# Performance work log

Measured on AMD Instinct MI355X. Metric: run time of the kernel, lower is better.

The kernel has to match this reference:

```python
import jax, jax.numpy as jnp
import numpy as np

INPUT_DIM = 16
LW = 128          # layerwidth
NB_LAYERS = 4
NB_X = 4096
NB_THETA = 128
PARAM_COUNT = INPUT_DIM * LW + LW + (NB_LAYERS - 1) * (LW * LW + LW) + LW + 1  # 51841


def setup_inputs() -> dict:
    k1, k2 = jax.random.split(jax.random.key(0))
    x = jax.random.normal(k1, (NB_X, INPUT_DIM), dtype=jnp.float32)
    theta = jax.random.normal(k2, (NB_THETA, PARAM_COUNT), dtype=jnp.float32)
    return {"x": x, "theta": theta}


def reference(x, theta):
    # x: [nb_x, input_dim], theta: [nb_theta, param_count]
    t = theta.shape[0]
    off = 0
    # first layer: W0 [t, LW, INPUT_DIM], b0 [t, LW]
    W0 = theta[:, off:off + INPUT_DIM * LW].reshape(t, LW, INPUT_DIM); off += INPUT_DIM * LW
    b0 = theta[:, off:off + LW]; off += LW
    h = jnp.tanh(jnp.einsum('thi,xi->txh', W0, x) + b0[:, None, :])  # [t, nb_x, LW]
    # hidden layers
    for _ in range(NB_LAYERS - 1):
        W = theta[:, off:off + LW * LW].reshape(t, LW, LW); off += LW * LW
        b = theta[:, off:off + LW]; off += LW
        h = jnp.tanh(jnp.einsum('tho,txo->txh', W, h) + b[:, None, :])
    # output layer: Wl [t, LW], bl [t, 1]
    Wl = theta[:, off:off + LW]; off += LW
    bl = theta[:, off:off + 1]
    out = jnp.einsum('th,txh->tx', Wl, h)[..., None] + bl[:, None, :]  # [t, nb_x, 1]
    return out
```

## Files before the change

kernel.cpp:

```cpp
#include <hip/hip_runtime.h>


#define IND      16
#define THREADS  1024
#define PARAMS   51841
#define SCALE    2.8853900817779268f

#define WS_W0    12582912
#define WS_SC    (WS_W0 + 128 * 8192)
#define WS_X     (WS_SC + 128 * 4096)
#define WS_XLO   (WS_X + 131072)
#define WS_TOTAL (WS_X + 262144)


#define LDS_B    98304
#define LDS_WL   (LDS_B + 1536)
#define LDS_SZ   (LDS_B + 2064)

typedef _Float16 f16x8 __attribute__((ext_vector_type(8)));
typedef _Float16 f16x4 __attribute__((ext_vector_type(4)));
typedef float    f32x16 __attribute__((ext_vector_type(16)));
typedef float    f32x4v __attribute__((ext_vector_type(4)));
typedef unsigned u32x2  __attribute__((ext_vector_type(2)));

union U4 { unsigned u[4]; f16x8 v; };

__device__ __forceinline__ unsigned tanh2pk(float z0, float z1) {
    const float e0 = __builtin_amdgcn_exp2f(z0);
    const float e1 = __builtin_amdgcn_exp2f(z1);
    const float y0 = __builtin_fmaf(__builtin_amdgcn_rcpf(1.0f + e0), -2.0f, 1.0f);
    const float y1 = __builtin_fmaf(__builtin_amdgcn_rcpf(1.0f + e1), -2.0f, 1.0f);
    return __builtin_bit_cast(unsigned, __builtin_amdgcn_cvt_pkrtz(y0, y1));
}

#define MFMA(A, B, C) __builtin_amdgcn_mfma_f32_32x32x16_f16((A), (B), (C), 0, 0, 0)

__device__ __forceinline__ void gload16(const void* g, void* l) {
    __builtin_amdgcn_global_load_lds(
        (const __attribute__((address_space(1))) void*)g,
        (__attribute__((address_space(3))) void*)l, 16, 0, 0);
}

__device__ __forceinline__ void conv8(const float* __restrict__ s, char* hidst,
                                      char* lodst, float scale) {
    float v[8];
    *reinterpret_cast<float4*>(v)     = *reinterpret_cast<const float4*>(s);
    *reinterpret_cast<float4*>(v + 4) = *reinterpret_cast<const float4*>(s + 4);
    f16x8 hi, lo;
#pragma unroll
    for (int i = 0; i < 8; ++i) {
        const float sv = v[i] * scale;
        hi[i] = (_Float16)sv;
        lo[i] = (_Float16)(sv - (float)hi[i]);
    }
    *reinterpret_cast<f16x8*>(hidst) = hi;
    *reinterpret_cast<f16x8*>(lodst) = lo;
}

__global__ __launch_bounds__(256)
void prep_kernel(const float* __restrict__ theta, const float* __restrict__ xin,
                 char* __restrict__ ws)
{
    const int b = blockIdx.x, tid = threadIdx.x;
    if (b < 3072) {
        const int t = b / 24, rem = b % 24, li = rem >> 3, hblk = rem & 7;
        const int h  = hblk * 16 + (tid >> 4);
        const int kc = (tid >> 1) & 7, kh = tid & 1;
        const float* src = theta + (size_t)t * PARAMS + 2176 + li * 16512
                         + h * 128 + kc * 16 + kh * 8;
        float v[8];
        *reinterpret_cast<float4*>(v)     = *reinterpret_cast<const float4*>(src);
        *reinterpret_cast<float4*>(v + 4) = *reinterpret_cast<const float4*>(src + 4);
        f16x8 p;
#pragma unroll
        for (int i = 0; i < 8; ++i) p[i] = (_Float16)(v[i] * SCALE);
        char* img = ws + ((size_t)(t * 3 + li) << 15);
        *reinterpret_cast<f16x8*>(img + ((h >> 5) * 8 + kc) * 1024
                                      + (kh * 32 + (h & 31)) * 16) = p;
    } else if (b < 3136) {
        const int gid = (b - 3072) * 256 + tid;
        const int t = gid >> 7, h = gid & 127;
        const float* src = theta + (size_t)t * PARAMS + h * IND;
        char* dst = ws + WS_W0 + (size_t)t * 8192 + h * 32;
        conv8(src,     dst,      dst + 4096,      SCALE);
        conv8(src + 8, dst + 16, dst + 4096 + 16, SCALE);
    } else if (b < 3264) {
        const int t = b - 3136;
        const float* th = theta + (size_t)t * PARAMS;
        float* base = reinterpret_cast<float*>(ws + WS_SC + (size_t)t * 4096);
        if (tid < 128) base[tid] = SCALE * th[2048 + tid];
        for (int k = tid; k < 384; k += 256)
            base[128 + k] = SCALE * th[2176 + (k >> 7) * 16512 + 16384 + (k & 127)];
        if (tid < 128) base[512 + tid] = th[51712 + tid];
        if (tid == 0)  base[640] = th[51840];
    } else {
        const int row = (b - 3264) * 256 + tid;
        const float* src = xin + (size_t)row * IND;
        char* hid = ws + WS_X   + (size_t)row * 32;
        char* lod = ws + WS_XLO + (size_t)row * 32;
        conv8(src,     hid,      lod,      1.0f);
        conv8(src + 8, hid + 16, lod + 16, 1.0f);
    }
}

__global__ __launch_bounds__(THREADS, 4)
void mlp_main(const char* __restrict__ ws, float* __restrict__ out)
{
    __shared__ __align__(16) char sL[LDS_SZ];

    const int tid = threadIdx.x, bid = blockIdx.x;
    const int sw  = (bid & 7) * 128 + (bid >> 3);
    const int t   = sw >> 3, xt = sw & 7;
    const int lane = tid & 63, w = tid >> 6, r31 = lane & 31, khalf = lane >> 5;
    const int bpa  = (lane ^ 32) << 2;
    (void)bpa;

    const float* __restrict__ wsc = reinterpret_cast<const float*>(
        ws + WS_SC + (size_t)t * 4096);

    {
        const char* img = ws + ((size_t)(t * 3) << 15);
#pragma unroll
        for (int c = 0; c < 6; ++c) {
            const int o = (c * 1024 + tid) * 16;
            gload16(img + o, sL + o);
        }
    }
    if (tid < 513)
        *reinterpret_cast<float*>(sL + LDS_B + tid * 4) = wsc[128 + tid];

    f32x16 acc[4];
    {
        const char* w0i = ws + WS_W0 + (size_t)t * 8192;
        const int ro = r31 * 32 + khalf * 16;
        const int xrow = (xt * 512 + w * 32) * 32;
        const f16x8 B0h = *reinterpret_cast<const f16x8*>(ws + WS_X   + xrow + ro);
        const f16x8 B0l = *reinterpret_cast<const f16x8*>(ws + WS_XLO + xrow + ro);
#pragma unroll
        for (int tt = 0; tt < 4; ++tt) {
#pragma unroll
            for (int g = 0; g < 4; ++g) {
                const f32x4v bv = *reinterpret_cast<const f32x4v*>(
                    wsc + tt * 32 + g * 8 + khalf * 4);
                acc[tt][4 * g + 0] = bv[0]; acc[tt][4 * g + 1] = bv[1];
                acc[tt][4 * g + 2] = bv[2]; acc[tt][4 * g + 3] = bv[3];
            }
            const f16x8 Ah = *reinterpret_cast<const f16x8*>(w0i + tt * 1024 + ro);
            const f16x8 Al = *reinterpret_cast<const f16x8*>(w0i + 4096 + tt * 1024 + ro);
            acc[tt] = MFMA(Al, B0h, acc[tt]);
            acc[tt] = MFMA(Ah, B0l, acc[tt]);
            acc[tt] = MFMA(Ah, B0h, acc[tt]);
        }
    }

    f16x8 Bf[8];
    auto activate_pack = [&]() {
#pragma unroll
        for (int tt = 0; tt < 4; ++tt) {
            unsigned P0[4], P1[4];
#pragma unroll
            for (int g = 0; g < 4; ++g) {
                P0[g] = tanh2pk(acc[tt][4 * g + 0], acc[tt][4 * g + 1]);
                P1[g] = tanh2pk(acc[tt][4 * g + 2], acc[tt][4 * g + 3]);
            }
#pragma unroll
            for (int j = 0; j < 2; ++j) {
#if __has_builtin(__builtin_amdgcn_permlane32_swap)
                const u32x2 r0 = __builtin_amdgcn_permlane32_swap(
                    P0[2 * j], P0[2 * j + 1], false, false);
                const u32x2 r1 = __builtin_amdgcn_permlane32_swap(
                    P1[2 * j], P1[2 * j + 1], false, false);
                U4 u;
                u.u[0] = r0[0]; u.u[1] = r1[0]; u.u[2] = r0[1]; u.u[3] = r1[1];
#else
                const unsigned s0 = khalf ? P0[2 * j] : P0[2 * j + 1];
                const unsigned s1 = khalf ? P1[2 * j] : P1[2 * j + 1];
                const unsigned q0 = (unsigned)__builtin_amdgcn_ds_bpermute(bpa, (int)s0);
                const unsigned q1 = (unsigned)__builtin_amdgcn_ds_bpermute(bpa, (int)s1);
                U4 u;
                u.u[0] = khalf ? q0 : P0[2 * j];
                u.u[1] = khalf ? q1 : P1[2 * j];
                u.u[2] = khalf ? P0[2 * j + 1] : q0;
                u.u[3] = khalf ? P1[2 * j + 1] : q1;
#endif
                Bf[2 * tt + j] = u.v;
            }
        }
    };
    activate_pack();

    __syncthreads();

#pragma unroll
    for (int l = 0; l < 3; ++l) {
        const char* wimg  = sL + l * 32768;
        const char* btab  = sL + LDS_B + l * 512;
        __builtin_amdgcn_s_setprio(1);
#pragma unroll
        for (int tt = 0; tt < 4; ++tt) {
#pragma unroll
            for (int g = 0; g < 4; ++g) {
                const f32x4v bv = *reinterpret_cast<const f32x4v*>(
                    btab + (tt * 32 + g * 8) * 4 + khalf * 16);
                acc[tt][4 * g + 0] = bv[0]; acc[tt][4 * g + 1] = bv[1];
                acc[tt][4 * g + 2] = bv[2]; acc[tt][4 * g + 3] = bv[3];
            }
#pragma unroll
            for (int kc = 0; kc < 8; ++kc) {
                const f16x8 a = *reinterpret_cast<const f16x8*>(
                    wimg + (tt * 8 + kc) * 1024 + lane * 16);
                acc[tt] = MFMA(a, Bf[kc], acc[tt]);
            }
        }
        __builtin_amdgcn_s_setprio(0);
        if (l < 2) activate_pack();
    }

    float s = 0.0f;
#pragma unroll
    for (int tt = 0; tt < 4; ++tt)
#pragma unroll
        for (int g = 0; g < 4; ++g) {
            const f32x4v wv = *reinterpret_cast<const f32x4v*>(
                sL + LDS_WL + (tt * 32 + g * 8) * 4 + khalf * 16);
#pragma unroll
            for (int q = 0; q < 4; ++q) {
                const float z = acc[tt][4 * g + q];
                const float e = __builtin_amdgcn_exp2f(z);
                const float y = __builtin_fmaf(
                    __builtin_amdgcn_rcpf(1.0f + e), -2.0f, 1.0f);
                s = __builtin_fmaf(y, wv[q], s);
            }
        }
    const float sp = __builtin_bit_cast(float,
        __builtin_amdgcn_ds_bpermute(bpa, __builtin_bit_cast(int, s)));
    const float res = s + sp + *reinterpret_cast<const float*>(sL + LDS_WL + 512);
    if (!khalf) out[(size_t)t * 4096 + xt * 512 + w * 32 + r31] = res;
}

__global__ __launch_bounds__(256, 1)
void mlp_kernel_fb(const float* __restrict__ xin,
                   const float* __restrict__ theta,
                   float* __restrict__ out)
{
    __shared__ __align__(16) _Float16 sH   [128 * 128];
    __shared__ __align__(16) _Float16 sWhi [128 * 128];
    __shared__ __align__(16) _Float16 sWlo [128 * 128];
    __shared__ __align__(16) _Float16 sX0hi[128 * IND];
    __shared__ __align__(16) _Float16 sX0lo[128 * IND];
    __shared__ __align__(16) _Float16 sW0hi[128 * IND];
    __shared__ __align__(16) _Float16 sW0lo[128 * IND];
    __shared__ float sB[2][128];
    __shared__ float sWl[129];

    const int tid = threadIdx.x;
    const int bid = blockIdx.x;
    const int sw  = (bid & 7) * 512 + (bid >> 3);
    const int t   = sw >> 5;
    const int xt  = sw & 31;
    const float* __restrict__ th = theta + (size_t)t * PARAMS;
    const float* __restrict__ xg = xin   + (size_t)xt * (128 * IND);

#pragma unroll
    for (int j = 0; j < 2; ++j) {
        const int flat = j * 1024 + tid * 4;
        const float4 v = *reinterpret_cast<const float4*>(xg + flat);
        _Float16 h0 = (_Float16)v.x, h1 = (_Float16)v.y, h2 = (_Float16)v.z, h3 = (_Float16)v.w;
        f16x4 ph = {h0, h1, h2, h3};
        f16x4 pl = {(_Float16)(v.x - (float)h0), (_Float16)(v.y - (float)h1),
                    (_Float16)(v.z - (float)h2), (_Float16)(v.w - (float)h3)};
        *reinterpret_cast<f16x4*>(&sX0hi[flat]) = ph;
        *reinterpret_cast<f16x4*>(&sX0lo[flat]) = pl;
    }
#pragma unroll
    for (int j = 0; j < 2; ++j) {
        const int flat = j * 1024 + tid * 4;
        const float a0 = th[flat], a1 = th[flat + 1], a2 = th[flat + 2], a3 = th[flat + 3];
        _Float16 h0 = (_Float16)a0, h1 = (_Float16)a1, h2 = (_Float16)a2, h3 = (_Float16)a3;
        f16x4 ph = {h0, h1, h2, h3};
        f16x4 pl = {(_Float16)(a0 - (float)h0), (_Float16)(a1 - (float)h1),
                    (_Float16)(a2 - (float)h2), (_Float16)(a3 - (float)h3)};
        *reinterpret_cast<f16x4*>(&sW0hi[flat]) = ph;
        *reinterpret_cast<f16x4*>(&sW0lo[flat]) = pl;
    }
    if (tid < 128) sB[0][tid] = th[IND * 128 + tid];
    __syncthreads();

    const int lane  = tid & 63;
    const int w     = tid >> 6;
    const int r31   = lane & 31;
    const int khalf = lane >> 5;
    const int hb    = (w >> 1) * 64;
    const int xb    = (w & 1) * 64;
    const int hA0 = hb + r31,  hA1 = hb + 32 + r31;
    const int xB0 = xb + r31,  xB1 = xb + 32 + r31;
    const int swzA0 = (hA0 & 15) << 4, swzA1 = (hA1 & 15) << 4;
    const int swzB0 = (xB0 & 15) << 4, swzB1 = (xB1 & 15) << 4;

    f32x16 acc[2][2];

    {
        const int kb = khalf * 16;
        f16x8 ah[2], al[2], bh[2], bl[2];
        ah[0] = *reinterpret_cast<const f16x8*>((const char*)sW0hi + hA0 * 32 + kb);
        ah[1] = *reinterpret_cast<const f16x8*>((const char*)sW0hi + hA1 * 32 + kb);
        al[0] = *reinterpret_cast<const f16x8*>((const char*)sW0lo + hA0 * 32 + kb);
        al[1] = *reinterpret_cast<const f16x8*>((const char*)sW0lo + hA1 * 32 + kb);
        bh[0] = *reinterpret_cast<const f16x8*>((const char*)sX0hi + xB0 * 32 + kb);
        bh[1] = *reinterpret_cast<const f16x8*>((const char*)sX0hi + xB1 * 32 + kb);
        bl[0] = *reinterpret_cast<const f16x8*>((const char*)sX0lo + xB0 * 32 + kb);
        bl[1] = *reinterpret_cast<const f16x8*>((const char*)sX0lo + xB1 * 32 + kb);
#pragma unroll
        for (int tt = 0; tt < 2; ++tt)
#pragma unroll
            for (int tx = 0; tx < 2; ++tx) {
                f32x16 a;
#pragma unroll
                for (int i = 0; i < 16; ++i) a[i] = 0.0f;
                a = MFMA(al[tt], bh[tx], a);
                a = MFMA(ah[tt], bl[tx], a);
                a = MFMA(ah[tt], bh[tx], a);
                acc[tt][tx] = a;
            }
    }

    auto epilogue = [&](const float* __restrict__ bb) {
#pragma unroll
        for (int tt = 0; tt < 2; ++tt)
#pragma unroll
            for (int tx = 0; tx < 2; ++tx) {
                const int xw  = xb + tx * 32 + r31;
                const int swz = (xw & 15) << 4;
#pragma unroll
                for (int g = 0; g < 4; ++g) {
                    const int hbase = hb + tt * 32 + g * 8 + khalf * 4;
                    f16x4 pk;
#pragma unroll
                    for (int q = 0; q < 4; ++q) {
                        const float v = acc[tt][tx][g * 4 + q] + bb[hbase + q];
                        pk[q] = (_Float16)(1.0f - 2.0f * __builtin_amdgcn_rcpf(
                            __builtin_amdgcn_exp2f(v * 2.8853900817779268f) + 1.0f));
                    }
                    *reinterpret_cast<f16x4*>((char*)sH + xw * 256 + ((hbase * 2) ^ swz)) = pk;
                }
            }
    };

    for (int l = 0; l < 3; ++l) {
        __syncthreads();
        const float* __restrict__ wsrc = th + 2176 + l * 16512;
#pragma unroll
        for (int j = 0; j < 16; ++j) {
            const int flat = j * 1024 + tid * 4;
            const int hrow = flat >> 7;
            const int o    = flat & 127;
            const float a0 = wsrc[flat], a1 = wsrc[flat + 1], a2 = wsrc[flat + 2], a3 = wsrc[flat + 3];
            _Float16 h0 = (_Float16)a0, h1 = (_Float16)a1, h2 = (_Float16)a2, h3 = (_Float16)a3;
            f16x4 ph = {h0, h1, h2, h3};
            f16x4 pl = {(_Float16)(a0 - (float)h0), (_Float16)(a1 - (float)h1),
                        (_Float16)(a2 - (float)h2), (_Float16)(a3 - (float)h3)};
            const int boff = hrow * 256 + ((o * 2) ^ ((hrow & 15) << 4));
            *reinterpret_cast<f16x4*>((char*)sWhi + boff) = ph;
            *reinterpret_cast<f16x4*>((char*)sWlo + boff) = pl;
        }
        if (tid < 128) sB[(l + 1) & 1][tid] = wsrc[128 * 128 + tid];
        if (l == 2) {
            if (tid < 128) sWl[tid] = th[51712 + tid];
            if (tid == 128) sWl[128] = th[51840];
        }

        epilogue(sB[l & 1]);
        __syncthreads();

#pragma unroll
        for (int tt = 0; tt < 2; ++tt)
#pragma unroll
            for (int tx = 0; tx < 2; ++tx)
#pragma unroll
                for (int i = 0; i < 16; ++i) acc[tt][tx][i] = 0.0f;
#pragma unroll
        for (int kc = 0; kc < 8; ++kc) {
            const int kb = kc * 32 + khalf * 16;
            f16x8 ah[2], al[2], bv[2];
            ah[0] = *reinterpret_cast<const f16x8*>((const char*)sWhi + hA0 * 256 + (kb ^ swzA0));
            ah[1] = *reinterpret_cast<const f16x8*>((const char*)sWhi + hA1 * 256 + (kb ^ swzA1));
            al[0] = *reinterpret_cast<const f16x8*>((const char*)sWlo + hA0 * 256 + (kb ^ swzA0));
            al[1] = *reinterpret_cast<const f16x8*>((const char*)sWlo + hA1 * 256 + (kb ^ swzA1));
            bv[0] = *reinterpret_cast<const f16x8*>((const char*)sH   + xB0 * 256 + (kb ^ swzB0));
            bv[1] = *reinterpret_cast<const f16x8*>((const char*)sH   + xB1 * 256 + (kb ^ swzB1));
#pragma unroll
            for (int tt = 0; tt < 2; ++tt)
#pragma unroll
                for (int tx = 0; tx < 2; ++tx) {
                    acc[tt][tx] = MFMA(al[tt], bv[tx], acc[tt][tx]);
                    acc[tt][tx] = MFMA(ah[tt], bv[tx], acc[tt][tx]);
                }
        }
    }

    __syncthreads();
    epilogue(sB[1]);
    __syncthreads();

    if (tid < 128) {
        const int r   = tid;
        const int swz = (r & 15) << 4;
        float s = 0.0f;
#pragma unroll
        for (int c = 0; c < 16; ++c) {
            const int hc = (c + r) & 15;
            const f16x8 hv = *reinterpret_cast<const f16x8*>(
                (const char*)sH + r * 256 + ((hc * 16) ^ swz));
#pragma unroll
            for (int q = 0; q < 8; ++q) s += (float)hv[q] * sWl[hc * 8 + q];
        }
        out[(size_t)t * 4096 + (size_t)xt * 128 + r] = s + sWl[128];
    }
}

extern "C" void kernel_launch(void* const* d_in, const int* in_sizes, int n_in,
                              void* d_out, int out_size, void* d_ws, size_t ws_size,
                              hipStream_t stream)
{
    const float* x     = (const float*)d_in[0];
    const float* theta = (const float*)d_in[1];
    float* out = (float*)d_out;

    if (ws_size >= (size_t)WS_TOTAL) {
        prep_kernel<<<dim3(3280), dim3(256), 0, stream>>>(theta, x, (char*)d_ws);
        mlp_main<<<dim3(1024), dim3(THREADS), 0, stream>>>((const char*)d_ws, out);
    } else {
        mlp_kernel_fb<<<dim3(4096), dim3(256), 0, stream>>>(x, theta, out);
    }
}
```

Before: 100.4 us.

## Interleave tanh activation of finished tiles with MFMAs of later tiles

Restructures the hidden-layer loop so that the tanh/pack of output tiles 0 and 1 is issued in the same loop as the MFMA chains for tiles 2 and 3. The activations are triple-buffered across FA/FB/FC fragments, so the next layer's input is produced while the current layer's matrix work is still in flight. The final layer similarly overlaps the output dot product with the remaining MFMAs. The aim is to hide transcendental ALU latency behind matrix-core work, at the cost of more live registers and more intricate scheduling.

```diff
diff --git a/kernel.cpp b/kernel.cpp
--- a/kernel.cpp
+++ b/kernel.cpp
@@ -129,109 +129,180 @@
     if (tid < 513)
         *reinterpret_cast<float*>(sL + LDS_B + tid * 4) = wsc[128 + tid];
 
-    f32x16 acc[4];
+    auto asm2 = [&](const unsigned* P0, const unsigned* P1, f16x8* dst) {
+#pragma unroll
+        for (int j = 0; j < 2; ++j) {
+#if __has_builtin(__builtin_amdgcn_permlane32_swap)
+            const u32x2 r0 = __builtin_amdgcn_permlane32_swap(
+                P0[2 * j], P0[2 * j + 1], false, false);
+            const u32x2 r1 = __builtin_amdgcn_permlane32_swap(
+                P1[2 * j], P1[2 * j + 1], false, false);
+            U4 u;
+            u.u[0] = r0[0]; u.u[1] = r1[0]; u.u[2] = r0[1]; u.u[3] = r1[1];
+#else
+            const unsigned s0 = khalf ? P0[2 * j] : P0[2 * j + 1];
+            const unsigned s1 = khalf ? P1[2 * j] : P1[2 * j + 1];
+            const unsigned q0 = (unsigned)__builtin_amdgcn_ds_bpermute(bpa, (int)s0);
+            const unsigned q1 = (unsigned)__builtin_amdgcn_ds_bpermute(bpa, (int)s1);
+            U4 u;
+            u.u[0] = khalf ? q0 : P0[2 * j];
+            u.u[1] = khalf ? q1 : P1[2 * j];
+            u.u[2] = khalf ? P0[2 * j + 1] : q0;
+            u.u[3] = khalf ? P1[2 * j + 1] : q1;
+#endif
+            dst[j] = u.v;
+        }
+    };
+    auto pack2 = [&](const f32x16& a, f16x8* dst) {
+        unsigned P0[4], P1[4];
+#pragma unroll
+        for (int g = 0; g < 4; ++g) {
+            P0[g] = tanh2pk(a[4 * g + 0], a[4 * g + 1]);
+            P1[g] = tanh2pk(a[4 * g + 2], a[4 * g + 3]);
+        }
+        asm2(P0, P1, dst);
+    };
+    auto biasin = [&](f32x16& a, const char* btab, int tt) {
+#pragma unroll
+        for (int g = 0; g < 4; ++g) {
+            const f32x4v bv = *reinterpret_cast<const f32x4v*>(
+                btab + (tt * 32 + g * 8) * 4 + khalf * 16);
+            a[4 * g + 0] = bv[0]; a[4 * g + 1] = bv[1];
+            a[4 * g + 2] = bv[2]; a[4 * g + 3] = bv[3];
+        }
+    };
+    auto mfma8 = [&](f32x16& a, const char* wimg, int tt,
+                     const f16x8* in0, const f16x8* in1) {
+#pragma unroll
+        for (int kc = 0; kc < 8; ++kc) {
+            const f16x8 av = *reinterpret_cast<const f16x8*>(
+                wimg + (tt * 8 + kc) * 1024 + lane * 16);
+            a = MFMA(av, kc < 4 ? in0[kc] : in1[kc - 4], a);
+        }
+    };
+    auto inter8 = [&](f32x16& a, const char* wimg, int tt,
+                      const f16x8* in0, const f16x8* in1,
+                      const f32x16& src, unsigned* P0, unsigned* P1) {
+#pragma unroll
+        for (int kc = 0; kc < 8; ++kc) {
+            const f16x8 av = *reinterpret_cast<const f16x8*>(
+                wimg + (tt * 8 + kc) * 1024 + lane * 16);
+            a = MFMA(av, kc < 4 ? in0[kc] : in1[kc - 4], a);
+            if (!(kc & 1)) {
+                const int g = kc >> 1;
+                P0[g] = tanh2pk(src[4 * g + 0], src[4 * g + 1]);
+                P1[g] = tanh2pk(src[4 * g + 2], src[4 * g + 3]);
+            }
+        }
+    };
+    auto inter8f = [&](f32x16& a, const char* wimg, int tt,
+                       const f16x8* in0, const f16x8* in1,
+                       const f32x16& src, int tts, float& s) {
+#pragma unroll
+        for (int kc = 0; kc < 8; ++kc) {
+            const f16x8 av = *reinterpret_cast<const f16x8*>(
+                wimg + (tt * 8 + kc) * 1024 + lane * 16);
+            a = MFMA(av, kc < 4 ? in0[kc] : in1[kc - 4], a);
+            if (!(kc & 1)) {
+                const int g = kc >> 1;
+                const f32x4v wv = *reinterpret_cast<const f32x4v*>(
+                    sL + LDS_WL + (tts * 32 + g * 8) * 4 + khalf * 16);
+#pragma unroll
+                for (int q = 0; q < 4; ++q) {
+                    const float z = src[4 * g + q];
+                    const float e = __builtin_amdgcn_exp2f(z);
+                    const float y = __builtin_fmaf(
+                        __builtin_amdgcn_rcpf(1.0f + e), -2.0f, 1.0f);
+                    s = __builtin_fmaf(y, wv[q], s);
+                }
+            }
+        }
+    };
+    auto fdot = [&](const f32x16& a, int tt, float& s) {
+#pragma unroll
+        for (int g = 0; g < 4; ++g) {
+            const f32x4v wv = *reinterpret_cast<const f32x4v*>(
+                sL + LDS_WL + (tt * 32 + g * 8) * 4 + khalf * 16);
+#pragma unroll
+            for (int q = 0; q < 4; ++q) {
+                const float z = a[4 * g + q];
+                const float e = __builtin_amdgcn_exp2f(z);
+                const float y = __builtin_fmaf(
+                    __builtin_amdgcn_rcpf(1.0f + e), -2.0f, 1.0f);
+                s = __builtin_fmaf(y, wv[q], s);
+            }
+        }
+    };
+
+    f16x8 FA[4], FB[4], FC[4];
     {
         const char* w0i = ws + WS_W0 + (size_t)t * 8192;
         const int ro = r31 * 32 + khalf * 16;
         const int xrow = (xt * 512 + w * 32) * 32;
         const f16x8 B0h = *reinterpret_cast<const f16x8*>(ws + WS_X   + xrow + ro);
         const f16x8 B0l = *reinterpret_cast<const f16x8*>(ws + WS_XLO + xrow + ro);
-#pragma unroll
-        for (int tt = 0; tt < 4; ++tt) {
+        auto l0tile = [&](f32x16& a, int tt) {
 #pragma unroll
             for (int g = 0; g < 4; ++g) {
                 const f32x4v bv = *reinterpret_cast<const f32x4v*>(
                     wsc + tt * 32 + g * 8 + khalf * 4);
-                acc[tt][4 * g + 0] = bv[0]; acc[tt][4 * g + 1] = bv[1];
-                acc[tt][4 * g + 2] = bv[2]; acc[tt][4 * g + 3] = bv[3];
+                a[4 * g + 0] = bv[0]; a[4 * g + 1] = bv[1];
+                a[4 * g + 2] = bv[2]; a[4 * g + 3] = bv[3];
             }
             const f16x8 Ah = *reinterpret_cast<const f16x8*>(w0i + tt * 1024 + ro);
             const f16x8 Al = *reinterpret_cast<const f16x8*>(w0i + 4096 + tt * 1024 + ro);
-            acc[tt] = MFMA(Al, B0h, acc[tt]);
-            acc[tt] = MFMA(Ah, B0l, acc[tt]);
-            acc[tt] = MFMA(Ah, B0h, acc[tt]);
-        }
-    }
-
-    f16x8 Bf[8];
-    auto activate_pack = [&]() {
-#pragma unroll
-        for (int tt = 0; tt < 4; ++tt) {
+            a = MFMA(Al, B0h, a);
+            a = MFMA(Ah, B0l, a);
+            a = MFMA(Ah, B0h, a);
+        };
+        f32x16 c0, c1;
+        l0tile(c0, 0); l0tile(c1, 1);
+        pack2(c0, &FA[0]); pack2(c1, &FA[2]);
+        l0tile(c0, 2); l0tile(c1, 3);
+        pack2(c0, &FB[0]); pack2(c1, &FB[2]);
+    }
+    __syncthreads();
+
+    auto hidden = [&](const char* wimg, const char* btab,
+                      f16x8* in0, f16x8* in1, f16x8* out0) {
+        f32x16 c0, c1, c2, c3;
+        __builtin_amdgcn_s_setprio(1);
+        biasin(c0, btab, 0); mfma8(c0, wimg, 0, in0, in1);
+        biasin(c1, btab, 1); mfma8(c1, wimg, 1, in0, in1);
+        {
             unsigned P0[4], P1[4];
-#pragma unroll
-            for (int g = 0; g < 4; ++g) {
-                P0[g] = tanh2pk(acc[tt][4 * g + 0], acc[tt][4 * g + 1]);
-                P1[g] = tanh2pk(acc[tt][4 * g + 2], acc[tt][4 * g + 3]);
-            }
-#pragma unroll
-            for (int j = 0; j < 2; ++j) {
-#if __has_builtin(__builtin_amdgcn_permlane32_swap)
-                const u32x2 r0 = __builtin_amdgcn_permlane32_swap(
-                    P0[2 * j], P0[2 * j + 1], false, false);
-                const u32x2 r1 = __builtin_amdgcn_permlane32_swap(
-                    P1[2 * j], P1[2 * j + 1], false, false);
-                U4 u;
-                u.u[0] = r0[0]; u.u[1] = r1[0]; u.u[2] = r0[1]; u.u[3] = r1[1];
-#else
-                const unsigned s0 = khalf ? P0[2 * j] : P0[2 * j + 1];
-                const unsigned s1 = khalf ? P1[2 * j] : P1[2 * j + 1];
-                const unsigned q0 = (unsigned)__builtin_amdgcn_ds_bpermute(bpa, (int)s0);
-                const unsigned q1 = (unsigned)__builtin_amdgcn_ds_bpermute(bpa, (int)s1);
-                U4 u;
-                u.u[0] = khalf ? q0 : P0[2 * j];
-                u.u[1] = khalf ? q1 : P1[2 * j];
-                u.u[2] = khalf ? P0[2 * j + 1] : q0;
-                u.u[3] = khalf ? P1[2 * j + 1] : q1;
-#endif
-                Bf[2 * tt + j] = u.v;
-            }
-        }
-    };
-    activate_pack();
-
-    __syncthreads();
-
-#pragma unroll
-    for (int l = 0; l < 3; ++l) {
-        const char* wimg  = sL + l * 32768;
-        const char* btab  = sL + LDS_B + l * 512;
+            biasin(c2, btab, 2);
+            inter8(c2, wimg, 2, in0, in1, c0, P0, P1);
+            asm2(P0, P1, out0 + 0);
+        }
+        {
+            unsigned P0[4], P1[4];
+            biasin(c3, btab, 3);
+            inter8(c3, wimg, 3, in0, in1, c1, P0, P1);
+            asm2(P0, P1, out0 + 2);
+        }
+        __builtin_amdgcn_s_setprio(0);
+        pack2(c2, in1 + 0);
+        pack2(c3, in1 + 2);
+    };
+
+    hidden(sL,         sL + LDS_B,        FA, FB, FC);
+    hidden(sL + 32768, sL + LDS_B + 512,  FC, FB, FA);
+
+    float s = 0.0f;
+    {
+        const char* wimg = sL + 65536;
+        const char* btab = sL + LDS_B + 1024;
+        f32x16 c0, c1, c2, c3;
         __builtin_amdgcn_s_setprio(1);
-#pragma unroll
-        for (int tt = 0; tt < 4; ++tt) {
-#pragma unroll
-            for (int g = 0; g < 4; ++g) {
-                const f32x4v bv = *reinterpret_cast<const f32x4v*>(
-                    btab + (tt * 32 + g * 8) * 4 + khalf * 16);
-                acc[tt][4 * g + 0] = bv[0]; acc[tt][4 * g + 1] = bv[1];
-                acc[tt][4 * g + 2] = bv[2]; acc[tt][4 * g + 3] = bv[3];
-            }
-#pragma unroll
-            for (int kc = 0; kc < 8; ++kc) {
-                const f16x8 a = *reinterpret_cast<const f16x8*>(
-                    wimg + (tt * 8 + kc) * 1024 + lane * 16);
-                acc[tt] = MFMA(a, Bf[kc], acc[tt]);
-            }
-        }
+        biasin(c0, btab, 0); mfma8(c0, wimg, 0, FA, FB);
+        biasin(c1, btab, 1); mfma8(c1, wimg, 1, FA, FB);
+        biasin(c2, btab, 2); inter8f(c2, wimg, 2, FA, FB, c0, 0, s);
+        biasin(c3, btab, 3); inter8f(c3, wimg, 3, FA, FB, c1, 1, s);
         __builtin_amdgcn_s_setprio(0);
-        if (l < 2) activate_pack();
-    }
-
-    float s = 0.0f;
-#pragma unroll
-    for (int tt = 0; tt < 4; ++tt)
-#pragma unroll
-        for (int g = 0; g < 4; ++g) {
-            const f32x4v wv = *reinterpret_cast<const f32x4v*>(
-                sL + LDS_WL + (tt * 32 + g * 8) * 4 + khalf * 16);
-#pragma unroll
-            for (int q = 0; q < 4; ++q) {
-                const float z = acc[tt][4 * g + q];
-                const float e = __builtin_amdgcn_exp2f(z);
-                const float y = __builtin_fmaf(
-                    __builtin_amdgcn_rcpf(1.0f + e), -2.0f, 1.0f);
-                s = __builtin_fmaf(y, wv[q], s);
-            }
-        }
+        fdot(c2, 2, s);
+        fdot(c3, 3, s);
+    }
     const float sp = __builtin_bit_cast(float,
         __builtin_amdgcn_ds_bpermute(bpa, __builtin_bit_cast(int, s)));
     const float res = s + sp + *reinterpret_cast<const float*>(sL + LDS_WL + 512);
```

After: 91.69 us. 8.6% less time.
